# Performance work log

Hardware: AMD Instinct MI355X
Metric: run time of the kernel (lower is better)

Reference implementation:

```python
import jax, jax.numpy as jnp
import numpy as np

LN2 = float(np.log(2.0))

def ssp(v):
    # PhysNet shifted softplus activation
    return jax.nn.softplus(v) - LN2

N, F, E, K, L = 50000, 128, 800000, 64, 3

def setup_inputs() -> dict:
    key = jax.random.key(0)
    ks = jax.random.split(key, 16)
    sc = 1.0 / np.sqrt(F)
    x = jax.random.normal(ks[0], (N, F), dtype=jnp.float32)
    rbf = jax.random.uniform(ks[1], (E, K), dtype=jnp.float32)
    idx_i = jnp.sort(jax.random.randint(ks[2], (E,), 0, N, dtype=jnp.int32))
    idx_j = jax.random.randint(ks[3], (E,), 0, N, dtype=jnp.int32)
    Wk2f = jax.random.normal(ks[4], (K, F), dtype=jnp.float32) / np.sqrt(K)
    Wi = jax.random.normal(ks[5], (F, F), dtype=jnp.float32) * sc
    bi = jnp.zeros((F,), jnp.float32)
    Wj = jax.random.normal(ks[6], (F, F), dtype=jnp.float32) * sc
    bj = jnp.zeros((F,), jnp.float32)
    Wr1 = jax.random.normal(ks[7], (L, F, F), dtype=jnp.float32) * sc
    br1 = jnp.zeros((L, F), jnp.float32)
    Wr2 = jax.random.normal(ks[8], (L, F, F), dtype=jnp.float32) * sc
    br2 = jnp.zeros((L, F), jnp.float32)
    Wf = jax.random.normal(ks[9], (F, F), dtype=jnp.float32) * sc
    bf = jnp.zeros((F,), jnp.float32)
    u = jnp.ones((F,), jnp.float32)
    return dict(x=x, rbf=rbf, Wk2f=Wk2f, Wi=Wi, bi=bi, Wj=Wj, bj=bj,
                Wr1=Wr1, br1=br1, Wr2=Wr2, br2=br2, Wf=Wf, bf=bf, u=u,
                idx_i=idx_i, idx_j=idx_j)

def reference(x, rbf, Wk2f, Wi, bi, Wj, bj, Wr1, br1, Wr2, br2, Wf, bf, u, idx_i, idx_j):
    xa = ssp(x)                                   # [N,F] (drop_rate=0 -> no dropout)
    g = rbf @ Wk2f                                # [E,F] rbf gate
    xi = ssp(xa @ Wi + bi)                        # [N,F]
    xj_all = ssp(xa @ Wj + bj)                    # [N,F]
    msgs = g * xj_all[idx_j]                      # [E,F] gather + gate
    xj = jax.ops.segment_sum(msgs, idx_i, num_segments=N)  # [N,F] scatter-reduce
    m = xi + xj
    for l in range(L):                            # PhysNet residual blocks
        y = ssp(m)
        m = m + ssp(y @ Wr1[l] + br1[l]) @ Wr2[l] + br2[l]
    m = ssp(m)
    return u * x + (m @ Wf + bf)
```

## Files before the change

### kernel.cpp

```cpp
#include <hip/hip_runtime.h>
#include <hip/hip_bf16.h>
#include <math.h>

typedef unsigned short u16;
typedef short bf16x8 __attribute__((ext_vector_type(8)));
typedef float f32x4 __attribute__((ext_vector_type(4)));

#define LN2F 0.693147180559945f

__device__ __forceinline__ float bf2f(u16 h) {
  union { unsigned int i; float f; } v; v.i = ((unsigned int)h) << 16; return v.f;
}
__device__ __forceinline__ u16 f2bf(float f) {
  union { float f; unsigned int i; } v; v.f = f;
  unsigned int x = v.i;
  return (u16)((x + 0x7fffu + ((x >> 16) & 1u)) >> 16);
}
__device__ __forceinline__ float sspf(float v) {
  return fmaxf(v, 0.0f) + __logf(1.0f + __expf(-fabsf(v))) - LN2F;
}
template<int MODE>
__device__ __forceinline__ float ldv(const void* p, size_t i) {
  if constexpr (MODE == 0) return bf2f(((const u16*)p)[i]);
  else                     return ((const float*)p)[i];
}

__global__ void probe_k(const u16* __restrict__ x, int* __restrict__ flag) {
  __shared__ int sf;
  if (threadIdx.x == 0) sf = 0;
  __syncthreads();
  int f = 0;
  for (int i = threadIdx.x; i < 4096; i += 256) {
    const unsigned e = (x[i] >> 7) & 0xFFu;
    if (e >= 0xC0u) f = 1;
  }
  if (f) atomicOr(&sf, 1);
  __syncthreads();
  if (threadIdx.x == 0) *flag = sf;
}

template<int NB>
__device__ __forceinline__ void copy_lin(const u16* __restrict__ g, u16* s, int tid) {
  constexpr int CH = NB / 16;
#pragma unroll
  for (int c = tid; c < CH; c += 256)
    *(bf16x8*)(s + (size_t)c * 8) = *(const bf16x8*)(g + (size_t)c * 8);
}

__device__ __forceinline__ void wload(const u16* __restrict__ g, bf16x8* w, int tid) {
#pragma unroll
  for (int p = 0; p < 8; ++p) w[p] = *(const bf16x8*)(g + (size_t)(tid + p * 256) * 8);
  if (tid < 128) w[8] = *(const bf16x8*)(g + (size_t)(2048 + tid) * 8);
}
__device__ __forceinline__ void wstore(u16* s, const bf16x8* w, int tid) {
#pragma unroll
  for (int p = 0; p < 8; ++p) *(bf16x8*)(s + (size_t)(tid + p * 256) * 8) = w[p];
  if (tid < 128) *(bf16x8*)(s + (size_t)(2048 + tid) * 8) = w[8];
}

template<int KSTEPS, int LDW>
__device__ __forceinline__ void mm_lds(const u16* sA, const u16* sW, f32x4* acc,
                                       int m16, int quad) {
#pragma unroll
  for (int s = 0; s < KSTEPS; ++s) {
    const int k0 = s * 32 + quad * 8;
    bf16x8 a = *(const bf16x8*)(sA + (size_t)m16 * LDW + k0);
#pragma unroll
    for (int t = 0; t < 8; ++t) {
      bf16x8 b = *(const bf16x8*)(sW + (size_t)(t * 16 + m16) * LDW + k0);
      acc[t] = __builtin_amdgcn_mfma_f32_16x16x32_bf16(a, b, acc[t], 0, 0, 0);
    }
  }
}

template<int MODE>
__global__ __launch_bounds__(256) void prep_k(
    const int* __restrict__ mode,
    const void* __restrict__ Wi, const void* __restrict__ Wj,
    const void* __restrict__ Wf, const void* __restrict__ Wk2f,
    const void* __restrict__ Wr1, const void* __restrict__ Wr2,
    u16* __restrict__ WT, int L)
{
  if (*mode != MODE) return;
  const int b = blockIdx.x, tid = threadIdx.x;
  constexpr size_t esz = (MODE == 0) ? 2 : 4;
  const void* src; u16* dst; int KD = 128, LDW = 136;
  if      (b == 0) { src = Wi;  dst = WT; }
  else if (b == 1) { src = Wj;  dst = WT + 17408; }
  else if (b == 2) { src = Wf;  dst = WT + 2 * 17408; }
  else if (b == 3) { src = Wk2f; dst = WT + (size_t)(3 + 2 * L) * 17408; KD = 64; LDW = 72; }
  else if (b < 4 + L) { int l = b - 4;     src = (const char*)Wr1 + (size_t)l * 16384 * esz; dst = WT + (size_t)(3 + l) * 17408; }
  else                { int l = b - 4 - L; src = (const char*)Wr2 + (size_t)l * 16384 * esz; dst = WT + (size_t)(3 + L + l) * 17408; }

  const int n  = tid & 127;
  const int kh = (tid >> 7) * (KD >> 1);
  for (int c = 0; c < (KD >> 4); ++c) {
    const int k0 = kh + c * 8;
    bf16x8 rv;
#pragma unroll
    for (int j = 0; j < 8; ++j)
      rv[j] = (short)f2bf(ldv<MODE>(src, (size_t)(k0 + j) * 128 + n));
    *(bf16x8*)(dst + (size_t)n * LDW + k0) = rv;
  }
}

template<int MODE>
__global__ __launch_bounds__(256) void in_k(
    const int* __restrict__ mode, const void* __restrict__ x,
    const u16* __restrict__ WiT, const u16* __restrict__ WjT,
    const void* __restrict__ bi, const void* __restrict__ bj,
    float* __restrict__ mb, u16* __restrict__ xjt, int N)
{
  if (*mode != MODE) return;
  __shared__ u16 sW[128 * 136];
  const int tid = threadIdx.x, lane = tid & 63, wave = tid >> 6;
  const int m16 = lane & 15, quad = lane >> 4;
  const int row_tile = blockIdx.x * 64 + wave * 16;
  int arow = row_tile + m16; if (arow >= N) arow = N - 1;

  bf16x8 af[4];
#pragma unroll
  for (int s = 0; s < 4; ++s) {
    const int k0 = s * 32 + quad * 8;
    if constexpr (MODE == 0) {
      bf16x8 raw = *(const bf16x8*)((const u16*)x + (size_t)arow * 128 + k0);
#pragma unroll
      for (int j = 0; j < 8; ++j) af[s][j] = (short)f2bf(sspf(bf2f((u16)raw[j])));
    } else {
      const float* ap = (const float*)x + (size_t)arow * 128 + k0;
      float4 lo = *(const float4*)ap, hi = *(const float4*)(ap + 4);
      float v[8] = {lo.x, lo.y, lo.z, lo.w, hi.x, hi.y, hi.z, hi.w};
#pragma unroll
      for (int j = 0; j < 8; ++j) af[s][j] = (short)f2bf(sspf(v[j]));
    }
  }

  copy_lin<128 * 136 * 2>(WiT, sW, tid);
  __syncthreads();
  f32x4 aI[8], aJ[8];
#pragma unroll
  for (int t = 0; t < 8; ++t) aI[t] = (f32x4){0.f, 0.f, 0.f, 0.f};
  bf16x8 w[9];
  wload(WjT, w, tid);
#pragma unroll
  for (int s = 0; s < 4; ++s) {
    const int k0 = s * 32 + quad * 8;
#pragma unroll
    for (int t = 0; t < 8; ++t) {
      bf16x8 b = *(const bf16x8*)(sW + (size_t)(t * 16 + m16) * 136 + k0);
      aI[t] = __builtin_amdgcn_mfma_f32_16x16x32_bf16(af[s], b, aI[t], 0, 0, 0);
    }
  }
  __syncthreads();
  wstore(sW, w, tid);
  __syncthreads();
#pragma unroll
  for (int t = 0; t < 8; ++t) aJ[t] = (f32x4){0.f, 0.f, 0.f, 0.f};
#pragma unroll
  for (int s = 0; s < 4; ++s) {
    const int k0 = s * 32 + quad * 8;
#pragma unroll
    for (int t = 0; t < 8; ++t) {
      bf16x8 b = *(const bf16x8*)(sW + (size_t)(t * 16 + m16) * 136 + k0);
      aJ[t] = __builtin_amdgcn_mfma_f32_16x16x32_bf16(af[s], b, aJ[t], 0, 0, 0);
    }
  }

#pragma unroll
  for (int t = 0; t < 8; ++t) {
    const int col = t * 16 + m16;
    const float biv = ldv<MODE>(bi, col), bjv = ldv<MODE>(bj, col);
#pragma unroll
    for (int r = 0; r < 4; ++r) {
      const int ro = row_tile + quad * 4 + r;
      if (ro >= N) continue;
      const size_t off = (size_t)ro * 128 + col;
      mb[off]  = sspf(aI[t][r] + biv);
      xjt[off] = f2bf(sspf(aJ[t][r] + bjv));
    }
  }
}

template<int MODE>
__global__ __launch_bounds__(256) void edge_k(
    const int* __restrict__ mode,
    const void* __restrict__ rbf, const u16* __restrict__ WkT,
    const u16* __restrict__ xj_all, const int* __restrict__ idx_i,
    const int* __restrict__ idx_j, float* __restrict__ mb, int E)
{
  if (*mode != MODE) return;
  __shared__ u16 sW[128 * 72];
  __shared__ u16 sXj[64][132];
  __shared__ int sIi[64], sIj[64];
  const int tid = threadIdx.x;
  const int e0 = blockIdx.x * 64;

  copy_lin<128 * 72 * 2>(WkT, sW, tid);
  if (tid < 64) {
    const int e = e0 + tid;
    sIi[tid] = (e < E) ? idx_i[e] : -1;
    sIj[tid] = (e < E) ? idx_j[e] : 0;
  }
  __syncthreads();

  {
    const int le = tid >> 4;
    const int c0 = (tid & 15) * 8;
#pragma unroll
    for (int p = 0; p < 4; ++p) {
      const int e = le + p * 16;
      const u16* src = xj_all + (size_t)sIj[e] * 128 + c0;
      ushort4 q0 = *(const ushort4*)src;
      ushort4 q1 = *(const ushort4*)(src + 4);
      *(ushort4*)&sXj[e][c0]     = q0;
      *(ushort4*)&sXj[e][c0 + 4] = q1;
    }
  }
  __syncthreads();

  const int lane = tid & 63, wave = tid >> 6;
  const int m16 = lane & 15, quad = lane >> 4;
  int erow = e0 + wave * 16 + m16; if (erow >= E) erow = E - 1;

  f32x4 acc[8];
#pragma unroll
  for (int t = 0; t < 8; ++t) acc[t] = (f32x4){0.f, 0.f, 0.f, 0.f};

#pragma unroll
  for (int s = 0; s < 2; ++s) {
    const int k0 = s * 32 + quad * 8;
    bf16x8 afr;
    if constexpr (MODE == 0) {
      afr = *(const bf16x8*)((const u16*)rbf + (size_t)erow * 64 + k0);
    } else {
      const float* ap = (const float*)rbf + (size_t)erow * 64 + k0;
      float4 lo = *(const float4*)ap, hi = *(const float4*)(ap + 4);
      afr[0] = f2bf(lo.x); afr[1] = f2bf(lo.y); afr[2] = f2bf(lo.z); afr[3] = f2bf(lo.w);
      afr[4] = f2bf(hi.x); afr[5] = f2bf(hi.y); afr[6] = f2bf(hi.z); afr[7] = f2bf(hi.w);
    }
#pragma unroll
    for (int t = 0; t < 8; ++t) {
      bf16x8 bfr = *(const bf16x8*)(sW + (size_t)(t * 16 + m16) * 72 + k0);
      acc[t] = __builtin_amdgcn_mfma_f32_16x16x32_bf16(afr, bfr, acc[t], 0, 0, 0);
    }
  }

#pragma unroll
  for (int t = 0; t < 8; ++t) {
    const int col = t * 16 + m16;
#pragma unroll
    for (int r = 0; r < 4; ++r) {
      const int le = wave * 16 + quad * 4 + r;
      float xv = (e0 + le < E) ? bf2f(sXj[le][col]) : 0.f;
      sXj[le][col] = f2bf(acc[t][r] * xv);
    }
  }
  __syncthreads();

  const int col = tid & 127;
  const int ebeg = (tid >> 7) * 32, eend = ebeg + 32;
  float sum = 0.f;
  int cur = sIi[ebeg];
  for (int le = ebeg; le < eend; ++le) {
    const int node = sIi[le];
    if (node != cur) {
      if (cur >= 0) atomicAdd(&mb[(size_t)cur * 128 + col], sum);
      sum = 0.f; cur = node;
    }
    sum += bf2f(sXj[le][col]);
  }
  if (cur >= 0) atomicAdd(&mb[(size_t)cur * 128 + col], sum);
}

template<int MODE>
__global__ __launch_bounds__(256) void resid_k(
    const int* __restrict__ mode, const float* __restrict__ mb,
    const u16* __restrict__ WT,
    const void* __restrict__ br1, const void* __restrict__ br2,
    const void* __restrict__ bfv, const void* __restrict__ x,
    const void* __restrict__ u, void* __restrict__ out, int N, int L)
{
  if (*mode != MODE) return;
  __shared__ u16 sW[128 * 136];
  __shared__ u16 sM[64 * 136];
  const int tid = threadIdx.x, lane = tid & 63, wave = tid >> 6;
  const int m16 = lane & 15, quad = lane >> 4;
  const int rbase = blockIdx.x * 64 + wave * 16 + quad * 4;
  u16* sMw = sM + (size_t)(wave * 16) * 136;

  f32x4 m[8];
#pragma unroll
  for (int t = 0; t < 8; ++t) {
    const int col = t * 16 + m16;
#pragma unroll
    for (int r = 0; r < 4; ++r) {
      int ro = rbase + r; if (ro >= N) ro = N - 1;
      m[t][r] = mb[(size_t)ro * 128 + col];
    }
  }

  const u16* W1T = WT + (size_t)3 * 17408;
  const u16* W2T = WT + (size_t)(3 + L) * 17408;
  bf16x8 w[9];

  for (int l = 0; l < L; ++l) {
    wload(W1T + (size_t)l * 17408, w, tid);
#pragma unroll
    for (int t = 0; t < 8; ++t) {
      const int col = t * 16 + m16;
#pragma unroll
      for (int r = 0; r < 4; ++r)
        sM[(size_t)(wave * 16 + quad * 4 + r) * 136 + col] = f2bf(sspf(m[t][r]));
    }
    wstore(sW, w, tid);
    __syncthreads();

    f32x4 a1[8];
#pragma unroll
    for (int t = 0; t < 8; ++t) a1[t] = (f32x4){0.f, 0.f, 0.f, 0.f};
    mm_lds<4, 136>(sMw, sW, a1, m16, quad);
    __syncthreads();

    wload(W2T + (size_t)l * 17408, w, tid);
#pragma unroll
    for (int t = 0; t < 8; ++t) {
      const int col = t * 16 + m16;
      const float b1v = ldv<MODE>(br1, (size_t)l * 128 + col);
#pragma unroll
      for (int r = 0; r < 4; ++r)
        sM[(size_t)(wave * 16 + quad * 4 + r) * 136 + col] = f2bf(sspf(a1[t][r] + b1v));
    }
    wstore(sW, w, tid);
    __syncthreads();

    mm_lds<4, 136>(sMw, sW, m, m16, quad);
#pragma unroll
    for (int t = 0; t < 8; ++t) {
      const float b2v = ldv<MODE>(br2, (size_t)l * 128 + t * 16 + m16);
#pragma unroll
      for (int r = 0; r < 4; ++r) m[t][r] += b2v;
    }
    __syncthreads();
  }

  wload(WT + (size_t)2 * 17408, w, tid);
#pragma unroll
  for (int t = 0; t < 8; ++t) {
    const int col = t * 16 + m16;
#pragma unroll
    for (int r = 0; r < 4; ++r)
      sM[(size_t)(wave * 16 + quad * 4 + r) * 136 + col] = f2bf(sspf(m[t][r]));
  }
  wstore(sW, w, tid);
  __syncthreads();

  f32x4 o[8];
#pragma unroll
  for (int t = 0; t < 8; ++t) o[t] = (f32x4){0.f, 0.f, 0.f, 0.f};
  mm_lds<4, 136>(sMw, sW, o, m16, quad);

#pragma unroll
  for (int t = 0; t < 8; ++t) {
    const int col = t * 16 + m16;
    const float bv = ldv<MODE>(bfv, col), uvv = ldv<MODE>(u, col);
#pragma unroll
    for (int r = 0; r < 4; ++r) {
      const int ro = rbase + r;
      if (ro >= N) continue;
      const size_t off = (size_t)ro * 128 + col;
      const float ov = uvv * ldv<MODE>(x, off) + o[t][r] + bv;
      if constexpr (MODE == 0) ((u16*)out)[off] = f2bf(ov);
      else                     ((float*)out)[off] = ov;
    }
  }
}

template<int MODE>
static void run_pipeline(const int* flag,
                         const void* x, const void* rbf, const void* Wk2f,
                         const void* Wi, const void* bi, const void* Wj, const void* bj,
                         const void* Wr1, const void* br1, const void* Wr2, const void* br2,
                         const void* Wf, const void* bfv, const void* uv,
                         const int* idx_i, const int* idx_j,
                         u16* WT, float* mb, u16* xjt, void* out,
                         int N, int E, int L, hipStream_t stream)
{
  const dim3 blk(256);
  const int gridN = (N + 63) / 64;
  const int gridE = (E + 63) / 64;

  prep_k<MODE><<<4 + 2 * L, blk, 0, stream>>>(flag, Wi, Wj, Wf, Wk2f, Wr1, Wr2, WT, L);
  in_k<MODE><<<gridN, blk, 0, stream>>>(flag, x, WT, WT + 17408, bi, bj, mb, xjt, N);
  edge_k<MODE><<<gridE, blk, 0, stream>>>(flag, rbf, WT + (size_t)(3 + 2 * L) * 17408,
                                          xjt, idx_i, idx_j, mb, E);
  resid_k<MODE><<<gridN, blk, 0, stream>>>(flag, mb, WT, br1, br2, bfv, x, uv, out, N, L);
}

extern "C" void kernel_launch(void* const* d_in, const int* in_sizes, int n_in,
                              void* d_out, int out_size, void* d_ws, size_t ws_size,
                              hipStream_t stream)
{
  const void* x    = d_in[0];
  const void* rbf  = d_in[1];
  const void* Wk2f = d_in[2];
  const void* Wi   = d_in[3];
  const void* bi   = d_in[4];
  const void* Wj   = d_in[5];
  const void* bj   = d_in[6];
  const void* Wr1  = d_in[7];
  const void* br1  = d_in[8];
  const void* Wr2  = d_in[9];
  const void* br2  = d_in[10];
  const void* Wf   = d_in[11];
  const void* bfv  = d_in[12];
  const void* uv   = d_in[13];
  const int* idx_i = (const int*)d_in[14];
  const int* idx_j = (const int*)d_in[15];

  const int N = in_sizes[0] / 128;
  const int E = in_sizes[14];
  const int L = in_sizes[7] / (128 * 128);

  int* flag = (int*)d_ws;
  char* wsb = (char*)d_ws + 16;
  const size_t avail = ws_size > 16 ? ws_size - 16 : 0;

  const size_t needW  = ((size_t)(3 + 2 * L) * 17408 + 9216) * 2;
  const size_t needWA = (needW + 255) & ~(size_t)255;
  u16* WT = (u16*)wsb;
  char* wsb2 = wsb + needWA;
  const size_t avail2 = (avail > needWA) ? avail - needWA : 0;

  const size_t needF = (size_t)N * 512;
  const size_t needH = (size_t)N * 256;

  float* mb0; u16* xjt0;
  if (avail2 >= needF + needH) { mb0 = (float*)wsb2; xjt0 = (u16*)(wsb2 + needF); }
  else                         { mb0 = (float*)wsb2; xjt0 = (u16*)d_out; }
  float* mb1; u16* xjt1;
  if (avail2 >= needF + needH)      { mb1 = (float*)wsb2;  xjt1 = (u16*)(wsb2 + needF); }
  else if (avail2 >= needF)         { mb1 = (float*)wsb2;  xjt1 = (u16*)d_out; }
  else                              { mb1 = (float*)d_out; xjt1 = (u16*)wsb2; }

  probe_k<<<1, 256, 0, stream>>>((const u16*)x, flag);
  run_pipeline<0>(flag, x, rbf, Wk2f, Wi, bi, Wj, bj, Wr1, br1, Wr2, br2,
                  Wf, bfv, uv, idx_i, idx_j, WT, mb0, xjt0, d_out, N, E, L, stream);
  run_pipeline<1>(flag, x, rbf, Wk2f, Wi, bi, Wj, bj, Wr1, br1, Wr2, br2,
                  Wf, bfv, uv, idx_i, idx_j, WT, mb1, xjt1, d_out, N, E, L, stream);
}
```

Baseline: 550.1 us.

## Make edge kernel persistent with double-buffered gather and carried segment sums

The edge kernel now launches a capped grid of persistent blocks, each walking a contiguous chunk of 64-edge tiles. Each block loads the Wk2f weights into shared memory once, double-buffers the gathered xj rows and edge indices, and prefetches the next tile's rbf and gather data into registers while the current tile is computed and reduced. Because idx_i is sorted, the running segment sum now carries across tiles, which cuts the number of atomic adds. In exchange the kernel uses more shared memory and registers, which may lower occupancy, and fewer blocks are in flight to hide the latency of the random gathers.

Result: slower. 574.7 us (+4.5%).

```diff
diff --git a/kernel.cpp b/kernel.cpp
--- a/kernel.cpp
+++ b/kernel.cpp
@@ -186,90 +186,122 @@
     const int* __restrict__ mode,
     const void* __restrict__ rbf, const u16* __restrict__ WkT,
     const u16* __restrict__ xj_all, const int* __restrict__ idx_i,
-    const int* __restrict__ idx_j, float* __restrict__ mb, int E)
+    const int* __restrict__ idx_j, float* __restrict__ mb,
+    int E, int ntiles, int chunk)
 {
   if (*mode != MODE) return;
   __shared__ u16 sW[128 * 72];
-  __shared__ u16 sXj[64][132];
-  __shared__ int sIi[64], sIj[64];
+  __shared__ u16 sXj[2][64 * 136];
+  __shared__ int sIi[2][64], sIj[2][64];
   const int tid = threadIdx.x;
-  const int e0 = blockIdx.x * 64;
-
-  copy_lin<128 * 72 * 2>(WkT, sW, tid);
-  if (tid < 64) {
-    const int e = e0 + tid;
-    sIi[tid] = (e < E) ? idx_i[e] : -1;
-    sIj[tid] = (e < E) ? idx_j[e] : 0;
-  }
-  __syncthreads();
-
-  {
-    const int le = tid >> 4;
-    const int c0 = (tid & 15) * 8;
-#pragma unroll
-    for (int p = 0; p < 4; ++p) {
-      const int e = le + p * 16;
-      const u16* src = xj_all + (size_t)sIj[e] * 128 + c0;
-      ushort4 q0 = *(const ushort4*)src;
-      ushort4 q1 = *(const ushort4*)(src + 4);
-      *(ushort4*)&sXj[e][c0]     = q0;
-      *(ushort4*)&sXj[e][c0 + 4] = q1;
-    }
-  }
-  __syncthreads();
+  const int tBeg = blockIdx.x * chunk;
+  const int tEnd = min(tBeg + chunk, ntiles);
+  if (tBeg >= ntiles) return;
 
   const int lane = tid & 63, wave = tid >> 6;
   const int m16 = lane & 15, quad = lane >> 4;
-  int erow = e0 + wave * 16 + m16; if (erow >= E) erow = E - 1;
-
-  f32x4 acc[8];
-#pragma unroll
-  for (int t = 0; t < 8; ++t) acc[t] = (f32x4){0.f, 0.f, 0.f, 0.f};
-
-#pragma unroll
-  for (int s = 0; s < 2; ++s) {
-    const int k0 = s * 32 + quad * 8;
-    bf16x8 afr;
+  const int gle = tid >> 4;
+  const int gc0 = (tid & 15) * 8;
+  const int scol = tid & 127;
+  const int sbeg = (tid >> 7) * 32;
+
+  bf16x8 rbH[2]; float4 rbF[4];
+  int ixi = -1, ixj = 0;
+
+  auto loadRbf = [&](int tt) {
+    int er = tt * 64 + wave * 16 + m16; if (er >= E) er = E - 1;
     if constexpr (MODE == 0) {
-      afr = *(const bf16x8*)((const u16*)rbf + (size_t)erow * 64 + k0);
+      const u16* p = (const u16*)rbf + (size_t)er * 64 + quad * 8;
+      rbH[0] = *(const bf16x8*)p;
+      rbH[1] = *(const bf16x8*)(p + 32);
     } else {
-      const float* ap = (const float*)rbf + (size_t)erow * 64 + k0;
-      float4 lo = *(const float4*)ap, hi = *(const float4*)(ap + 4);
-      afr[0] = f2bf(lo.x); afr[1] = f2bf(lo.y); afr[2] = f2bf(lo.z); afr[3] = f2bf(lo.w);
-      afr[4] = f2bf(hi.x); afr[5] = f2bf(hi.y); afr[6] = f2bf(hi.z); afr[7] = f2bf(hi.w);
-    }
-#pragma unroll
-    for (int t = 0; t < 8; ++t) {
-      bf16x8 bfr = *(const bf16x8*)(sW + (size_t)(t * 16 + m16) * 72 + k0);
-      acc[t] = __builtin_amdgcn_mfma_f32_16x16x32_bf16(afr, bfr, acc[t], 0, 0, 0);
-    }
-  }
-
-#pragma unroll
-  for (int t = 0; t < 8; ++t) {
-    const int col = t * 16 + m16;
-#pragma unroll
-    for (int r = 0; r < 4; ++r) {
-      const int le = wave * 16 + quad * 4 + r;
-      float xv = (e0 + le < E) ? bf2f(sXj[le][col]) : 0.f;
-      sXj[le][col] = f2bf(acc[t][r] * xv);
-    }
-  }
-  __syncthreads();
-
-  const int col = tid & 127;
-  const int ebeg = (tid >> 7) * 32, eend = ebeg + 32;
-  float sum = 0.f;
-  int cur = sIi[ebeg];
-  for (int le = ebeg; le < eend; ++le) {
-    const int node = sIi[le];
-    if (node != cur) {
-      if (cur >= 0) atomicAdd(&mb[(size_t)cur * 128 + col], sum);
-      sum = 0.f; cur = node;
-    }
-    sum += bf2f(sXj[le][col]);
-  }
-  if (cur >= 0) atomicAdd(&mb[(size_t)cur * 128 + col], sum);
+      const float* p = (const float*)rbf + (size_t)er * 64 + quad * 8;
+      rbF[0] = *(const float4*)p;        rbF[1] = *(const float4*)(p + 4);
+      rbF[2] = *(const float4*)(p + 32); rbF[3] = *(const float4*)(p + 36);
+    }
+  };
+  auto loadIdx = [&](int tt) {
+    if (tid < 64) {
+      const int e = tt * 64 + tid;
+      ixi = (e < E) ? idx_i[e] : -1;
+      ixj = (e < E) ? idx_j[e] : 0;
+    }
+  };
+
+  copy_lin<128 * 72 * 2>(WkT, sW, tid);
+  loadIdx(tBeg);
+  if (tid < 64) { sIi[0][tid] = ixi; sIj[0][tid] = ixj; }
+  __syncthreads();
+  bf16x8 g[4];
+#pragma unroll
+  for (int p = 0; p < 4; ++p)
+    g[p] = *(const bf16x8*)(xj_all + (size_t)sIj[0][gle + p * 16] * 128 + gc0);
+  loadRbf(tBeg);
+  loadIdx(min(tBeg + 1, tEnd - 1));
+#pragma unroll
+  for (int p = 0; p < 4; ++p)
+    *(bf16x8*)(&sXj[0][(size_t)(gle + p * 16) * 136 + gc0]) = g[p];
+
+  int curNode = -1; float sum = 0.f;
+  int cur = 0;
+  for (int t = tBeg; t < tEnd; ++t, cur ^= 1) {
+    const int nxt = cur ^ 1;
+    __syncthreads();
+    f32x4 acc[8];
+#pragma unroll
+    for (int t8 = 0; t8 < 8; ++t8) acc[t8] = (f32x4){0.f, 0.f, 0.f, 0.f};
+#pragma unroll
+    for (int s = 0; s < 2; ++s) {
+      bf16x8 af;
+      if constexpr (MODE == 0) af = rbH[s];
+      else {
+        const float4 lo = rbF[2 * s], hi = rbF[2 * s + 1];
+        af[0] = f2bf(lo.x); af[1] = f2bf(lo.y); af[2] = f2bf(lo.z); af[3] = f2bf(lo.w);
+        af[4] = f2bf(hi.x); af[5] = f2bf(hi.y); af[6] = f2bf(hi.z); af[7] = f2bf(hi.w);
+      }
+      const int k0 = s * 32 + quad * 8;
+#pragma unroll
+      for (int t8 = 0; t8 < 8; ++t8) {
+        bf16x8 b = *(const bf16x8*)(sW + (size_t)(t8 * 16 + m16) * 72 + k0);
+        acc[t8] = __builtin_amdgcn_mfma_f32_16x16x32_bf16(af, b, acc[t8], 0, 0, 0);
+      }
+    }
+    if (tid < 64) { sIi[nxt][tid] = ixi; sIj[nxt][tid] = ixj; }
+#pragma unroll
+    for (int t8 = 0; t8 < 8; ++t8) {
+      const int col = t8 * 16 + m16;
+#pragma unroll
+      for (int r = 0; r < 4; ++r) {
+        const int le = wave * 16 + quad * 4 + r;
+        const float xv = (t * 64 + le < E) ? bf2f(sXj[cur][(size_t)le * 136 + col]) : 0.f;
+        sXj[cur][(size_t)le * 136 + col] = f2bf(acc[t8][r] * xv);
+      }
+    }
+    __syncthreads();
+    const bool more = (t + 1 < tEnd);
+    if (more) {
+#pragma unroll
+      for (int p = 0; p < 4; ++p)
+        g[p] = *(const bf16x8*)(xj_all + (size_t)sIj[nxt][gle + p * 16] * 128 + gc0);
+      loadRbf(t + 1);
+      loadIdx(min(t + 2, tEnd - 1));
+    }
+#pragma unroll 4
+    for (int r = 0; r < 32; ++r) {
+      const int node = sIi[cur][sbeg + r];
+      if (node != curNode) {
+        if (curNode >= 0) atomicAdd(&mb[(size_t)curNode * 128 + scol], sum);
+        sum = 0.f; curNode = node;
+      }
+      sum += bf2f(sXj[cur][(size_t)(sbeg + r) * 136 + scol]);
+    }
+    if (more) {
+#pragma unroll
+      for (int p = 0; p < 4; ++p)
+        *(bf16x8*)(&sXj[nxt][(size_t)(gle + p * 16) * 136 + gc0]) = g[p];
+    }
+  }
+  if (curNode >= 0) atomicAdd(&mb[(size_t)curNode * 128 + scol], sum);
 }
 
 template<int MODE>
@@ -387,12 +419,17 @@
 {
   const dim3 blk(256);
   const int gridN = (N + 63) / 64;
-  const int gridE = (E + 63) / 64;
 
   prep_k<MODE><<<4 + 2 * L, blk, 0, stream>>>(flag, Wi, Wj, Wf, Wk2f, Wr1, Wr2, WT, L);
   in_k<MODE><<<gridN, blk, 0, stream>>>(flag, x, WT, WT + 17408, bi, bj, mb, xjt, N);
-  edge_k<MODE><<<gridE, blk, 0, stream>>>(flag, rbf, WT + (size_t)(3 + 2 * L) * 17408,
-                                          xjt, idx_i, idx_j, mb, E);
+
+  const int ntiles = (E + 63) >> 6;
+  int nblk = ntiles < 768 ? ntiles : 768;
+  const int chunk = (ntiles + nblk - 1) / nblk;
+  nblk = (ntiles + chunk - 1) / chunk;
+  edge_k<MODE><<<nblk, blk, 0, stream>>>(flag, rbf, WT + (size_t)(3 + 2 * L) * 17408,
+                                         xjt, idx_i, idx_j, mb, E, ntiles, chunk);
+
   resid_k<MODE><<<gridN, blk, 0, stream>>>(flag, mb, WT, br1, br2, bfv, x, uv, out, N, L);
 }
 
```

## Gather xj rows directly into registers and issue all edge loads up front

Applied to the files above, without the earlier changes.

The edge kernel now loads idx_j per lane and gathers xj_all values straight into registers in MFMA output layout. This replaces the shared-memory staging pass and one of its barriers. The weight tile and rbf fragments are also loaded into registers before any barrier, so all global loads are in flight together before the LDS store and sync. The gather now uses scalar 2-byte loads, 32 per lane, instead of 16-byte vector loads, which trades memory coalescing for fewer barriers and shorter serial latency.

After: 510.6 us. -7.2%, faster.

```diff
diff --git a/kernel.cpp b/kernel.cpp
--- a/kernel.cpp
+++ b/kernel.cpp
@@ -190,58 +190,69 @@
 {
   if (*mode != MODE) return;
   __shared__ u16 sW[128 * 72];
-  __shared__ u16 sXj[64][132];
-  __shared__ int sIi[64], sIj[64];
+  __shared__ u16 sMsg[64][132];
+  __shared__ int sIi[64];
   const int tid = threadIdx.x;
   const int e0 = blockIdx.x * 64;
-
-  copy_lin<128 * 72 * 2>(WkT, sW, tid);
-  if (tid < 64) {
-    const int e = e0 + tid;
-    sIi[tid] = (e < E) ? idx_i[e] : -1;
-    sIj[tid] = (e < E) ? idx_j[e] : 0;
-  }
-  __syncthreads();
-
-  {
-    const int le = tid >> 4;
-    const int c0 = (tid & 15) * 8;
-#pragma unroll
-    for (int p = 0; p < 4; ++p) {
-      const int e = le + p * 16;
-      const u16* src = xj_all + (size_t)sIj[e] * 128 + c0;
-      ushort4 q0 = *(const ushort4*)src;
-      ushort4 q1 = *(const ushort4*)(src + 4);
-      *(ushort4*)&sXj[e][c0]     = q0;
-      *(ushort4*)&sXj[e][c0 + 4] = q1;
-    }
-  }
-  __syncthreads();
-
   const int lane = tid & 63, wave = tid >> 6;
   const int m16 = lane & 15, quad = lane >> 4;
-  int erow = e0 + wave * 16 + m16; if (erow >= E) erow = E - 1;
+  const int lebase = wave * 16 + quad * 4;
+
+  if (tid < 64) sIi[tid] = (e0 + tid < E) ? idx_i[e0 + tid] : -1;
+  int jrow[4];
+#pragma unroll
+  for (int r = 0; r < 4; ++r) {
+    const int e = e0 + lebase + r;
+    jrow[r] = (e < E) ? idx_j[e] : 0;
+  }
+
+  bf16x8 w[5];
+#pragma unroll
+  for (int p = 0; p < 4; ++p) w[p] = *(const bf16x8*)(WkT + (size_t)(tid + p * 256) * 8);
+  if (tid < 128) w[4] = *(const bf16x8*)(WkT + (size_t)(1024 + tid) * 8);
+
+  int er = e0 + wave * 16 + m16; if (er >= E) er = E - 1;
+  bf16x8 rbH[2]; float4 rbF[4];
+  if constexpr (MODE == 0) {
+    const u16* p = (const u16*)rbf + (size_t)er * 64 + quad * 8;
+    rbH[0] = *(const bf16x8*)p;
+    rbH[1] = *(const bf16x8*)(p + 32);
+  } else {
+    const float* p = (const float*)rbf + (size_t)er * 64 + quad * 8;
+    rbF[0] = *(const float4*)p;        rbF[1] = *(const float4*)(p + 4);
+    rbF[2] = *(const float4*)(p + 32); rbF[3] = *(const float4*)(p + 36);
+  }
+
+  u16 xg[8][4];
+#pragma unroll
+  for (int r = 0; r < 4; ++r) {
+    const u16* xr = xj_all + (size_t)jrow[r] * 128 + m16;
+#pragma unroll
+    for (int t = 0; t < 8; ++t) xg[t][r] = xr[t * 16];
+  }
+
+#pragma unroll
+  for (int p = 0; p < 4; ++p) *(bf16x8*)(sW + (size_t)(tid + p * 256) * 8) = w[p];
+  if (tid < 128) *(bf16x8*)(sW + (size_t)(1024 + tid) * 8) = w[4];
+  __syncthreads();
 
   f32x4 acc[8];
 #pragma unroll
   for (int t = 0; t < 8; ++t) acc[t] = (f32x4){0.f, 0.f, 0.f, 0.f};
-
 #pragma unroll
   for (int s = 0; s < 2; ++s) {
+    bf16x8 af;
+    if constexpr (MODE == 0) af = rbH[s];
+    else {
+      const float4 lo = rbF[2 * s], hi = rbF[2 * s + 1];
+      af[0] = f2bf(lo.x); af[1] = f2bf(lo.y); af[2] = f2bf(lo.z); af[3] = f2bf(lo.w);
+      af[4] = f2bf(hi.x); af[5] = f2bf(hi.y); af[6] = f2bf(hi.z); af[7] = f2bf(hi.w);
+    }
     const int k0 = s * 32 + quad * 8;
-    bf16x8 afr;
-    if constexpr (MODE == 0) {
-      afr = *(const bf16x8*)((const u16*)rbf + (size_t)erow * 64 + k0);
-    } else {
-      const float* ap = (const float*)rbf + (size_t)erow * 64 + k0;
-      float4 lo = *(const float4*)ap, hi = *(const float4*)(ap + 4);
-      afr[0] = f2bf(lo.x); afr[1] = f2bf(lo.y); afr[2] = f2bf(lo.z); afr[3] = f2bf(lo.w);
-      afr[4] = f2bf(hi.x); afr[5] = f2bf(hi.y); afr[6] = f2bf(hi.z); afr[7] = f2bf(hi.w);
-    }
-#pragma unroll
-    for (int t = 0; t < 8; ++t) {
-      bf16x8 bfr = *(const bf16x8*)(sW + (size_t)(t * 16 + m16) * 72 + k0);
-      acc[t] = __builtin_amdgcn_mfma_f32_16x16x32_bf16(afr, bfr, acc[t], 0, 0, 0);
+#pragma unroll
+    for (int t = 0; t < 8; ++t) {
+      bf16x8 b = *(const bf16x8*)(sW + (size_t)(t * 16 + m16) * 72 + k0);
+      acc[t] = __builtin_amdgcn_mfma_f32_16x16x32_bf16(af, b, acc[t], 0, 0, 0);
     }
   }
 
@@ -250,26 +261,26 @@
     const int col = t * 16 + m16;
 #pragma unroll
     for (int r = 0; r < 4; ++r) {
-      const int le = wave * 16 + quad * 4 + r;
-      float xv = (e0 + le < E) ? bf2f(sXj[le][col]) : 0.f;
-      sXj[le][col] = f2bf(acc[t][r] * xv);
-    }
-  }
-  __syncthreads();
-
-  const int col = tid & 127;
-  const int ebeg = (tid >> 7) * 32, eend = ebeg + 32;
+      const float xvf = (e0 + lebase + r < E) ? bf2f(xg[t][r]) : 0.f;
+      sMsg[lebase + r][col] = f2bf(acc[t][r] * xvf);
+    }
+  }
+  __syncthreads();
+
+  const int scol = tid & 127;
+  const int sbeg = (tid >> 7) * 32;
   float sum = 0.f;
-  int cur = sIi[ebeg];
-  for (int le = ebeg; le < eend; ++le) {
-    const int node = sIi[le];
+  int cur = sIi[sbeg];
+#pragma unroll 4
+  for (int r = 0; r < 32; ++r) {
+    const int node = sIi[sbeg + r];
     if (node != cur) {
-      if (cur >= 0) atomicAdd(&mb[(size_t)cur * 128 + col], sum);
+      if (cur >= 0) atomicAdd(&mb[(size_t)cur * 128 + scol], sum);
       sum = 0.f; cur = node;
     }
-    sum += bf2f(sXj[le][col]);
-  }
-  if (cur >= 0) atomicAdd(&mb[(size_t)cur * 128 + col], sum);
+    sum += bf2f(sMsg[sbeg + r][scol]);
+  }
+  if (cur >= 0) atomicAdd(&mb[(size_t)cur * 128 + scol], sum);
 }
 
 template<int MODE>
```
